# Kernel optimization log

Hardware: AMD Instinct MI355X
Metric: run time of the kernel (lower is better)

The kernel has to match this reference:

```python
import jax, jax.numpy as jnp
import numpy as np

N = 20000   # nodes per graph batch
E = 160000  # edges
G = 128     # graphs in batch
F = 114     # node feature dim (num_features == num_features_xd)
H = 10      # GAT heads
HF = F * H  # 1140


def setup_inputs() -> dict:
    key = jax.random.key(0)
    ks = jax.random.split(key, 64)
    ki = iter(range(64))
    def rn(shape, scale=0.05):
        return jax.random.normal(ks[next(ki)], shape, dtype=jnp.float32) * scale
    inp = {}
    inp["x1"] = jax.random.normal(ks[next(ki)], (N, F), dtype=jnp.float32)
    inp["edge_index1"] = jax.random.randint(ks[next(ki)], (2, E), 0, N)
    inp["batch1"] = jnp.sort(jax.random.randint(ks[next(ki)], (N,), 0, G))
    inp["x2"] = jax.random.normal(ks[next(ki)], (N, F), dtype=jnp.float32)
    inp["edge_index2"] = jax.random.randint(ks[next(ki)], (2, E), 0, N)
    inp["batch2"] = jnp.sort(jax.random.randint(ks[next(ki)], (N,), 0, G))
    inp["target"] = jax.random.normal(ks[next(ki)], (G, 1000), dtype=jnp.float32)
    for p in ("p1", "p2"):
        inp[p + "_gatW"] = rn((F, HF))
        inp[p + "_att_src"] = rn((H, F))
        inp[p + "_att_dst"] = rn((H, F))
        inp[p + "_gatb"] = rn((HF,))
        inp[p + "_gcnW"] = rn((HF, HF))
        inp[p + "_gcnb"] = rn((HF,))
        inp[p + "_fcg1W"] = rn((2 * HF, 1000))
        inp[p + "_fcg1b"] = rn((1000,))
        inp[p + "_fcg2W"] = rn((1000, 64))
        inp[p + "_fcg2b"] = rn((64,))
    inp["fcxtW"] = rn((1000, 128)); inp["fcxtb"] = rn((128,))
    inp["fc1W"] = rn((256, 128)); inp["fc1b"] = rn((128,))
    inp["fc2W"] = rn((128, 32)); inp["fc2b"] = rn((32,))
    inp["outW"] = rn((32, 1)); inp["outb"] = rn((1,))
    return inp


def lrelu(v):
    return jax.nn.leaky_relu(v, 0.01)  # nn.LeakyReLU default slope


def gat_conv(x, src, dst, W, att_src, att_dst, b):
    # PyG GATConv (concat heads, add_self_loops handled by caller)
    h = (x @ W).reshape(N, H, F)                     # [N,H,F]
    a_s = jnp.sum(h * att_src[None], axis=-1)        # [N,H]
    a_d = jnp.sum(h * att_dst[None], axis=-1)        # [N,H]
    e = jax.nn.leaky_relu(a_s[src] + a_d[dst], 0.2)  # [E',H]
    m = jax.ops.segment_max(e, dst, num_segments=N)
    ex = jnp.exp(e - m[dst])
    den = jax.ops.segment_sum(ex, dst, num_segments=N)
    alpha = ex / den[dst]                            # softmax over incoming edges
    out = jax.ops.segment_sum(alpha[:, :, None] * h[src], dst, num_segments=N)
    return out.reshape(N, HF) + b


def gcn_conv(x, src, dst, W, b):
    # PyG GCNConv with self loops (added by caller), symmetric normalization
    deg = jax.ops.segment_sum(jnp.ones_like(dst, dtype=x.dtype), dst, num_segments=N)
    dinv = jax.lax.rsqrt(jnp.maximum(deg, 1.0))
    h = x @ W                                        # [N,HF]
    msg = (dinv[src] * dinv[dst])[:, None] * h[src]
    return jax.ops.segment_sum(msg, dst, num_segments=N) + b


def branch(x, edge_index, batch, gatW, a_s, a_d, gatb, gcnW, gcnb, f1W, f1b, f2W, f2b):
    loop = jnp.arange(N, dtype=edge_index.dtype)
    src = jnp.concatenate([edge_index[0], loop])
    dst = jnp.concatenate([edge_index[1], loop])
    h = lrelu(gat_conv(x, src, dst, gatW, a_s, a_d, gatb))
    h = lrelu(gcn_conv(h, src, dst, gcnW, gcnb))
    mx = jax.ops.segment_max(h, batch, num_segments=G)
    mx = jnp.where(jnp.isfinite(mx), mx, 0.0)        # guard empty graphs
    cnt = jax.ops.segment_sum(jnp.ones((N,), h.dtype), batch, num_segments=G)
    mean = jax.ops.segment_sum(h, batch, num_segments=G) / jnp.maximum(cnt, 1.0)[:, None]
    g = jnp.concatenate([mx, mean], axis=1)          # [G, 2*HF]
    g = lrelu(g @ f1W + f1b)                         # dropout is identity at eval
    return g @ f2W + f2b                             # [G, 64]


def reference(x1, edge_index1, batch1, x2, edge_index2, batch2, target,
              p1_gatW, p1_att_src, p1_att_dst, p1_gatb, p1_gcnW, p1_gcnb,
              p1_fcg1W, p1_fcg1b, p1_fcg2W, p1_fcg2b,
              p2_gatW, p2_att_src, p2_att_dst, p2_gatb, p2_gcnW, p2_gcnb,
              p2_fcg1W, p2_fcg1b, p2_fcg2W, p2_fcg2b,
              fcxtW, fcxtb, fc1W, fc1b, fc2W, fc2b, outW, outb):
    g1 = branch(x1, edge_index1, batch1, p1_gatW, p1_att_src, p1_att_dst, p1_gatb,
                p1_gcnW, p1_gcnb, p1_fcg1W, p1_fcg1b, p1_fcg2W, p1_fcg2b)
    g2 = branch(x2, edge_index2, batch2, p2_gatW, p2_att_src, p2_att_dst, p2_gatb,
                p2_gcnW, p2_gcnb, p2_fcg1W, p2_fcg1b, p2_fcg2W, p2_fcg2b)
    xd = jnp.concatenate([g1, g2], axis=1)           # [G,128]
    xt = target.reshape(-1, 1000) @ fcxtW + fcxtb    # [G,128]
    xc = jnp.concatenate([xd, xt], axis=1)           # [G,256]
    xc = lrelu(xc @ fc1W + fc1b)
    xc = lrelu(xc @ fc2W + fc2b)
    return xc @ outW + outb                          # [G,1]
```

## Files before the change

### kernel.cpp

```cpp
#include <hip/hip_runtime.h>
#include <cstddef>
#include <cstdint>

#define NN 20000
#define EE 160000
#define EPRIME 180000
#define GG 128
#define FF 114
#define HH 10
#define HFD 1140
#define KP 1152
#define F1K 2280
#define F1KS 18
#define F1KC 128
#define NSCB 79

typedef unsigned short ushort_t;
typedef __attribute__((ext_vector_type(8))) short bf16x8;
typedef __attribute__((ext_vector_type(4))) float f32x4;

static constexpr size_t REL  = (size_t)NN * KP;
static constexpr size_t ZREL = (size_t)10 * NN * 128;

static inline int cdiv(int a, int b) { return (a + b - 1) / b; }


__device__ __forceinline__ ushort_t f2bf(float v) {
    union { float f; unsigned u; } c; c.f = v;
    unsigned u = c.u;
    unsigned r = (u + 0x7fffu + ((u >> 16) & 1u)) >> 16;
    return (ushort_t)r;
}
__device__ __forceinline__ float bf2f(ushort_t h) {
    union { unsigned u; float f; } c; c.u = ((unsigned)h) << 16;
    return c.f;
}

__device__ __forceinline__ void gload16(const void* g, const ushort_t* l) {
    __builtin_amdgcn_global_load_lds(
        (const __attribute__((address_space(1))) unsigned int*)g,
        (__attribute__((address_space(3))) unsigned int*)l, 16, 0, 0);
}


__global__ void k_init(int* __restrict__ deg, int* __restrict__ gstart, int* __restrict__ gend) {
    int br = blockIdx.y;
    int i = blockIdx.x * blockDim.x + threadIdx.x;
    if (i < NN) deg[br * NN + i] = 1;
    if (i < GG) { gstart[br * GG + i] = NN; gend[br * GG + i] = 0; }
}

__global__ void k_count(const int* __restrict__ ei0, const int* __restrict__ ei1,
                        int* __restrict__ deg) {
    int br = blockIdx.y;
    const int* ei = br ? ei1 : ei0;
    int i = blockIdx.x * blockDim.x + threadIdx.x;
    if (i < EE) atomicAdd(&deg[br * NN + ei[EE + i]], 1);
}

__global__ void k_scan1(const int* __restrict__ deg, int* __restrict__ offs, int* __restrict__ bsum) {
    __shared__ int tmp[256];
    int br = blockIdx.y;
    deg += br * NN; offs += br * (NN + 1); bsum += br * 128;
    int b = blockIdx.x, tid = threadIdx.x;
    int i = b * 256 + tid;
    int v = (i < NN) ? deg[i] : 0;
    tmp[tid] = v;
    __syncthreads();
#pragma unroll
    for (int off = 1; off < 256; off <<= 1) {
        int t = (tid >= off) ? tmp[tid - off] : 0;
        __syncthreads();
        tmp[tid] += t;
        __syncthreads();
    }
    if (i < NN) offs[i + 1] = tmp[tid];
    if (tid == 255) bsum[b] = tmp[255];
}

__global__ void k_scan2(int* __restrict__ bsum) {
    __shared__ int tmp[128];
    bsum += blockIdx.y * 128;
    int tid = threadIdx.x;
    int v = (tid < NSCB) ? bsum[tid] : 0;
    tmp[tid] = v;
    __syncthreads();
#pragma unroll
    for (int off = 1; off < 128; off <<= 1) {
        int t = (tid >= off) ? tmp[tid - off] : 0;
        __syncthreads();
        tmp[tid] += t;
        __syncthreads();
    }
    if (tid < NSCB) bsum[tid] = tmp[tid] - v;
}

__global__ void k_scan3prep(int* __restrict__ offs, const int* __restrict__ bsum,
                            int* __restrict__ cursor, const int* __restrict__ deg,
                            float* __restrict__ dinv,
                            const int* __restrict__ batch0, const int* __restrict__ batch1,
                            int* __restrict__ gstart, int* __restrict__ gend) {
    int br = blockIdx.y;
    offs += br * (NN + 1); bsum += br * 128; cursor += br * NN;
    deg += br * NN; dinv += br * NN;
    const int* batch = br ? batch1 : batch0;
    gstart += br * GG; gend += br * GG;
    int i = blockIdx.x * 256 + threadIdx.x;
    if (i < NN) {
        int o = offs[i + 1] + bsum[i >> 8];
        offs[i + 1] = o;
        cursor[i] = o - deg[i];
        dinv[i] = rsqrtf((float)deg[i]);
        int b = batch[i];
        atomicMin(&gstart[b], i);
        atomicMax(&gend[b], i + 1);
    }
    if (i == 0) offs[0] = 0;
}

__global__ void k_fill(const int* __restrict__ ei0, const int* __restrict__ ei1,
                       int* __restrict__ cursor, int* __restrict__ csr) {
    int br = blockIdx.y;
    const int* ei = br ? ei1 : ei0;
    cursor += br * NN; csr += (size_t)br * EPRIME;
    int i = blockIdx.x * blockDim.x + threadIdx.x;
    if (i < EPRIME) {
        int s, d;
        if (i < EE) { s = ei[i]; d = ei[EE + i]; }
        else        { s = i - EE; d = s; }
        int pos = atomicAdd(&cursor[d], 1);
        csr[pos] = s;
    }
}


__global__ void k_split_x(const float* __restrict__ x0, const float* __restrict__ x1,
                          ushort_t* __restrict__ xb) {
    int br = blockIdx.y;
    const float* x = br ? x1 : x0;
    xb += (size_t)br * REL;
    int idx = blockIdx.x * 256 + threadIdx.x;
    if (idx >= NN * 128) return;
    int n = idx >> 7, k = idx & 127;
    float v = (k < FF) ? x[(size_t)n * FF + k] : 0.f;
    xb[idx] = f2bf(v);
}

__global__ __launch_bounds__(256) void k_tbf(const float* __restrict__ W0, const float* __restrict__ W1,
                                             int K, int Nc, int Kpad, ushort_t* __restrict__ T) {
    __shared__ float tile[64][65];
    int br = blockIdx.z;
    const float* W = br ? W1 : W0;
    T += (size_t)br * KP * KP;
    int kb = blockIdx.x * 64;
    int nb = blockIdx.y * 64;
    int c = threadIdx.x & 63, r4 = threadIdx.x >> 6;
#pragma unroll
    for (int rr = 0; rr < 16; ++rr) {
        int r = r4 * 16 + rr;
        int gk = kb + r, gn = nb + c;
        tile[r][c] = (gk < K && gn < Nc) ? W[(size_t)gk * Nc + gn] : 0.f;
    }
    __syncthreads();
#pragma unroll
    for (int rr = 0; rr < 16; ++rr) {
        int r = r4 * 16 + rr;
        int gn = nb + r, gk = kb + c;
        T[(size_t)gn * Kpad + gk] = f2bf(tile[c][r]);
    }
}

__global__ __launch_bounds__(256) void k_wgtT(const float* __restrict__ W0, const float* __restrict__ W1,
                                              ushort_t* __restrict__ WgT) {
    __shared__ float tile[64][65];
    int y = blockIdx.z;
    int br = y / 10, h = y - 10 * br;
    const float* W = br ? W1 : W0;
    ushort_t* T = WgT + ((size_t)br * 10 + h) * 128 * 128;
    int kb = blockIdx.x * 64, cb = blockIdx.y * 64;
    int c = threadIdx.x & 63, r4 = threadIdx.x >> 6;
#pragma unroll
    for (int rr = 0; rr < 16; ++rr) {
        int r = r4 * 16 + rr;
        int gk = kb + r, gc = cb + c;
        tile[r][c] = (gk < FF && gc < FF) ? W[(size_t)gk * HFD + h * FF + gc] : 0.f;
    }
    __syncthreads();
#pragma unroll
    for (int rr = 0; rr < 16; ++rr) {
        int r = r4 * 16 + rr;
        int gc2 = cb + r, gk2 = kb + c;
        T[(size_t)gc2 * 128 + gk2] = f2bf(tile[c][r]);
    }
}

__global__ void k_vsd(const float* __restrict__ W0, const float* __restrict__ W1,
                      const float* __restrict__ as0, const float* __restrict__ as1,
                      const float* __restrict__ ad0, const float* __restrict__ ad1,
                      float* __restrict__ Vs, float* __restrict__ Vd) {
    int br = blockIdx.y;
    const float* W = br ? W1 : W0;
    const float* asrc = br ? as1 : as0;
    const float* adst = br ? ad1 : ad0;
    int idx = blockIdx.x * 256 + threadIdx.x;
    if (idx >= 1280) return;
    int k = idx / 10, h = idx - 10 * (idx / 10);
    float vs = 0.f, vd = 0.f;
    if (k < FF) {
        const float* wrow = W + (size_t)k * HFD + h * FF;
        const float* s = asrc + h * FF;
        const float* d = adst + h * FF;
        for (int f = 0; f < FF; ++f) { vs += wrow[f] * s[f]; vd += wrow[f] * d[f]; }
    }
    Vs[br * 1280 + idx] = vs;
    Vd[br * 1280 + idx] = vd;
}

__global__ void k_att2(const ushort_t* __restrict__ xbase,
                       const float* __restrict__ Vs, const float* __restrict__ Vd,
                       float* __restrict__ as_, float* __restrict__ ad_) {
    int br = blockIdx.y;
    const ushort_t* xb = xbase + (size_t)br * REL;
    const float* vs = Vs + br * 1280;
    const float* vd = Vd + br * 1280;
    as_ += (size_t)br * NN * HH; ad_ += (size_t)br * NN * HH;
    int id = blockIdx.x * blockDim.x + threadIdx.x;
    if (id >= NN * HH) return;
    int n = id / HH, h = id - HH * (id / HH);
    const ushort_t* row = xb + (size_t)n * 128;
    float as = 0.f, ad = 0.f;
    for (int k = 0; k < FF; k += 2) {
        unsigned qq = *(const unsigned*)(row + k);
        float v0 = bf2f((ushort_t)(qq & 0xffffu));
        float v1 = bf2f((ushort_t)(qq >> 16));
        as += v0 * vs[k * 10 + h] + v1 * vs[(k + 1) * 10 + h];
        ad += v0 * vd[k * 10 + h] + v1 * vd[(k + 1) * 10 + h];
    }
    as_[id] = as;
    ad_[id] = ad;
}


template <int NU>
__device__ __forceinline__ void gax_grp(
    int eg, int end, int lane, float my_ad,
    const int* __restrict__ csr, const float* __restrict__ as_,
    const ushort_t* __restrict__ xb,
    float& den, float acc[HH][2]) {
    int s[NU]; float ex[NU];
#pragma unroll
    for (int u = 0; u < NU; ++u) {
        int idx = eg + u; if (idx > end - 1) idx = end - 1;
        s[u] = csr[idx];
    }
#pragma unroll
    for (int u = 0; u < NU; ++u) {
        float e = 0.f;
        if (lane < HH) {
            float t = as_[s[u] * HH + lane] + my_ad;
            t = (t >= 0.f) ? t : 0.2f * t;
            e = __expf(t);
            if (eg + u >= end) e = 0.f;
        }
        ex[u] = e;
        den += e;
    }
    unsigned xv[NU];
#pragma unroll
    for (int u = 0; u < NU; ++u)
        xv[u] = *(const unsigned*)(xb + (size_t)s[u] * 128 + 2 * lane);
#pragma unroll
    for (int u = 0; u < NU; ++u) {
        float x0 = bf2f((ushort_t)(xv[u] & 0xffffu));
        float x1 = bf2f((ushort_t)(xv[u] >> 16));
#pragma unroll
        for (int h = 0; h < HH; ++h) {
            float w = __shfl(ex[u], h, 64);
            acc[h][0] += w * x0;
            acc[h][1] += w * x1;
        }
    }
}

__global__ __launch_bounds__(256) void gat_aggx(
    const ushort_t* __restrict__ xbase,
    const float* __restrict__ as_, const float* __restrict__ ad_,
    const int* __restrict__ offs, const int* __restrict__ csr,
    ushort_t* __restrict__ Z) {
    int br = blockIdx.y;
    const ushort_t* xb = xbase + (size_t)br * REL;
    as_ += (size_t)br * NN * HH; ad_ += (size_t)br * NN * HH;
    offs += br * (NN + 1); csr += (size_t)br * EPRIME;
    ushort_t* Zb = Z + (size_t)br * ZREL;

    int lane = threadIdx.x & 63;
    int n = blockIdx.x * 4 + (threadIdx.x >> 6);
    if (n >= NN) return;
    int beg = offs[n], end = offs[n + 1];
    float my_ad = (lane < HH) ? ad_[n * HH + lane] : 0.f;

    float den = 0.f;
    float acc[HH][2];
#pragma unroll
    for (int h = 0; h < HH; ++h) { acc[h][0] = 0.f; acc[h][1] = 0.f; }

    int eg = beg;
    for (; eg + 8 <= end; eg += 8)
        gax_grp<8>(eg, end, lane, my_ad, csr, as_, xb, den, acc);
    for (; eg < end; eg += 4)
        gax_grp<4>(eg, end, lane, my_ad, csr, as_, xb, den, acc);

#pragma unroll
    for (int h = 0; h < HH; ++h) {
        float d = __shfl(den, h, 64);
        float inv = 1.f / d;
        unsigned pk = (unsigned)f2bf(acc[h][0] * inv)
                    | ((unsigned)f2bf(acc[h][1] * inv) << 16);
        *(unsigned*)(Zb + ((size_t)h * NN + n) * 128 + 2 * lane) = pk;
    }
}


__global__ __launch_bounds__(256) void mfma_hgemm(
    const ushort_t* __restrict__ Zbase, const ushort_t* __restrict__ WgT,
    const float* __restrict__ b0, const float* __restrict__ b1,
    ushort_t* __restrict__ Cbase) {
    __shared__ __align__(16) ushort_t lds[2 * 8192];
    int y = blockIdx.y;
    int br = y / 10, h = y - 10 * br;
    const ushort_t* A = Zbase + (size_t)br * ZREL + (size_t)h * NN * 128;
    const ushort_t* Bt = WgT + ((size_t)br * 10 + h) * 128 * 128;
    const float* bias = (br ? b1 : b0) + h * FF;
    ushort_t* Cb = Cbase + (size_t)br * REL;

    const int tid = threadIdx.x;
    const int lane = tid & 63;
    const int w = tid >> 6;
    const int wr = w >> 1, wc = w & 1;

    int nwg = gridDim.x;
    int q = nwg >> 3, r8 = nwg & 7;
    int xcd = blockIdx.x & 7, sidx = blockIdx.x >> 3;
    int wg = (xcd < r8 ? xcd * (q + 1) : r8 * (q + 1) + (xcd - r8) * q) + sidx;

    int row0 = wg * 128; if (row0 > NN - 128) row0 = NN - 128;

    f32x4 acc[4][4];
#pragma unroll
    for (int i = 0; i < 4; ++i)
#pragma unroll
        for (int j = 0; j < 4; ++j) acc[i][j] = (f32x4){0.f, 0.f, 0.f, 0.f};

    const char* pA[2]; const char* pB[2];
    unsigned ldsoff[2];
#pragma unroll
    for (int i = 0; i < 2; ++i) {
        int c = (w * 2 + i) * 64 + lane;
        int kg = c >> 7, r = c & 127;
        pA[i] = (const char*)A + (size_t)(row0 + r) * 256 + kg * 16;
        pB[i] = (const char*)Bt + (size_t)r * 256 + kg * 16;
        ldsoff[i] = (w * 2 + i) * 512;
    }
    const int kgf = lane >> 4, r15 = lane & 15;

    auto STAGE = [&](int buf, int ks) {
        size_t kb = (size_t)ks * 64;
        unsigned bo = buf ? 8192u : 0u;
#pragma unroll
        for (int i = 0; i < 2; ++i) {
            gload16(pA[i] + kb, lds + bo + 0 + ldsoff[i]);
            gload16(pB[i] + kb, lds + bo + 4096 + ldsoff[i]);
        }
    };

    STAGE(0, 0);
    asm volatile("s_waitcnt vmcnt(0)" ::: "memory");
    __syncthreads();
    int cur = 0;

    for (int ks = 0; ks < 4; ++ks) {
        if (ks + 1 < 4) STAGE(cur ^ 1, ks + 1);
        const ushort_t* lb = lds + (cur ? 8192u : 0u);
        bf16x8 ah[4], bh[4];
#pragma unroll
        for (int i = 0; i < 4; ++i) {
            int ra = wr * 64 + i * 16 + r15;
            int rb = wc * 64 + i * 16 + r15;
            ah[i] = *(const bf16x8*)(lb + 0 + kgf * 1024 + ra * 8);
            bh[i] = *(const bf16x8*)(lb + 4096 + kgf * 1024 + rb * 8);
        }
#pragma unroll
        for (int i = 0; i < 4; ++i)
#pragma unroll
            for (int j = 0; j < 4; ++j)
                acc[i][j] = __builtin_amdgcn_mfma_f32_16x16x32_bf16(ah[i], bh[j], acc[i][j], 0, 0, 0);
        asm volatile("s_waitcnt vmcnt(0)" ::: "memory");
        __syncthreads();
        cur ^= 1;
    }

    const int g4 = lane >> 4;
#pragma unroll
    for (int i = 0; i < 4; ++i)
#pragma unroll
        for (int j = 0; j < 4; ++j) {
            int c = wc * 64 + j * 16 + r15;
#pragma unroll
            for (int reg = 0; reg < 4; ++reg) {
                int r = row0 + wr * 64 + i * 16 + g4 * 4 + reg;
                int gc = h * FF + c;
                if (c < FF) {
                    float v = acc[i][j][reg] + bias[c];
                    v = (v >= 0.f) ? v : 0.01f * v;
                    Cb[(size_t)r * KP + gc] = f2bf(v);
                } else if (h == 9 && gc < KP) {
                    Cb[(size_t)r * KP + gc] = 0;
                }
            }
        }
}


__global__ __launch_bounds__(256) void mfma_gemm(
    const ushort_t* __restrict__ Abase, const ushort_t* __restrict__ Btbase,
    int lda, int ldb, int M, int Nreal, int ksteps, int ncb,
    ushort_t* __restrict__ Cbase, int ldcs) {
    __shared__ __align__(16) ushort_t lds[3 * 8192];
    const int br = blockIdx.y;
    const ushort_t* A = Abase + (size_t)br * REL;
    const ushort_t* Bt = Btbase + (size_t)br * KP * KP;
    ushort_t* Cb = Cbase + (size_t)br * ZREL;

    const int tid = threadIdx.x;
    const int lane = tid & 63;
    const int w = tid >> 6;
    const int wr = w >> 1, wc = w & 1;

    int nwg = gridDim.x;
    int q = nwg >> 3, r8 = nwg & 7;
    int xcd = blockIdx.x & 7, sidx = blockIdx.x >> 3;
    int wg = (xcd < r8 ? xcd * (q + 1) : r8 * (q + 1) + (xcd - r8) * q) + sidx;
    int brow = wg / ncb, bcol = wg - brow * ncb;

    int row0 = brow * 128; if (row0 > M - 128) row0 = M - 128;
    const int col0 = bcol * 128;

    f32x4 acc[4][4];
#pragma unroll
    for (int i = 0; i < 4; ++i)
#pragma unroll
        for (int j = 0; j < 4; ++j) acc[i][j] = (f32x4){0.f, 0.f, 0.f, 0.f};

    const size_t ldaB = (size_t)lda * 2, ldbB = (size_t)ldb * 2;
    const char* pA[2]; const char* pB[2];
    unsigned ldsoff[2];
#pragma unroll
    for (int i = 0; i < 2; ++i) {
        int c = (w * 2 + i) * 64 + lane;
        int kg = c >> 7, r = c & 127;
        pA[i] = (const char*)A + (size_t)(row0 + r) * ldaB + kg * 16;
        pB[i] = (const char*)Bt + (size_t)(col0 + r) * ldbB + kg * 16;
        ldsoff[i] = (w * 2 + i) * 512;
    }
    const int kgf = lane >> 4, r15 = lane & 15;

    auto STAGE = [&](int stg, int ks) {
        size_t kb = (size_t)ks * 64;
        unsigned bo = (unsigned)stg * 8192u;
#pragma unroll
        for (int i = 0; i < 2; ++i) {
            gload16(pA[i] + kb, lds + bo + 0 + ldsoff[i]);
            gload16(pB[i] + kb, lds + bo + 4096 + ldsoff[i]);
        }
    };

    STAGE(0, 0);
    STAGE(1, 1);
    asm volatile("s_waitcnt vmcnt(4)" ::: "memory");
    __builtin_amdgcn_s_barrier();
    __builtin_amdgcn_sched_barrier(0);

    for (int ks = 0; ks < ksteps; ++ks) {
        if (ks + 2 < ksteps) STAGE((ks + 2) % 3, ks + 2);
        const ushort_t* lb = lds + (ks % 3) * 8192;
        bf16x8 ah[4], bh[4];
#pragma unroll
        for (int i = 0; i < 4; ++i) {
            int ra = wr * 64 + i * 16 + r15;
            int rb = wc * 64 + i * 16 + r15;
            ah[i] = *(const bf16x8*)(lb + 0 + kgf * 1024 + ra * 8);
            bh[i] = *(const bf16x8*)(lb + 4096 + kgf * 1024 + rb * 8);
        }
#pragma unroll
        for (int i = 0; i < 4; ++i)
#pragma unroll
            for (int j = 0; j < 4; ++j)
                acc[i][j] = __builtin_amdgcn_mfma_f32_16x16x32_bf16(ah[i], bh[j], acc[i][j], 0, 0, 0);
        if (ks + 2 < ksteps) { asm volatile("s_waitcnt vmcnt(4)" ::: "memory"); }
        else                 { asm volatile("s_waitcnt vmcnt(0)" ::: "memory"); }
        __builtin_amdgcn_s_barrier();
        __builtin_amdgcn_sched_barrier(0);
    }

    const int g4 = lane >> 4;
#pragma unroll
    for (int i = 0; i < 4; ++i)
#pragma unroll
        for (int j = 0; j < 4; ++j) {
            int c = col0 + wc * 64 + j * 16 + r15;
#pragma unroll
            for (int reg = 0; reg < 4; ++reg) {
                int r = row0 + wr * 64 + i * 16 + g4 * 4 + reg;
                if (r < M) {
                    float v = (c < Nreal) ? acc[i][j][reg] : 0.f;
                    Cb[(size_t)r * ldcs + c] = f2bf(v);
                }
            }
        }
}


template <int NU>
__device__ __forceinline__ void gcn_grp(
    int eg, int end, float di,
    const int* __restrict__ csr, const float* __restrict__ dinv,
    const ushort_t* __restrict__ h2s,
    float& a0, float& a1) {
    int s[NU]; float w[NU];
#pragma unroll
    for (int u = 0; u < NU; ++u) {
        int idx = eg + u; if (idx > end - 1) idx = end - 1;
        s[u] = csr[idx];
    }
#pragma unroll
    for (int u = 0; u < NU; ++u) {
        float ww = dinv[s[u]] * di;
        w[u] = (eg + u < end) ? ww : 0.f;
    }
    unsigned qv[NU];
#pragma unroll
    for (int u = 0; u < NU; ++u)
        qv[u] = *(const unsigned*)(h2s + (size_t)s[u] * KP);
#pragma unroll
    for (int u = 0; u < NU; ++u) {
        a0 += w[u] * bf2f((ushort_t)(qv[u] & 0xffffu));
        a1 += w[u] * bf2f((ushort_t)(qv[u] >> 16));
    }
}

__global__ __launch_bounds__(256) void gcn_agg(
    const ushort_t* __restrict__ h2base, const int* __restrict__ offs, const int* __restrict__ csr,
    const float* __restrict__ dinv,
    const float* __restrict__ b0, const float* __restrict__ b1,
    ushort_t* __restrict__ outbase) {
    int br = blockIdx.z;
    int tile = blockIdx.y;
    const ushort_t* h2b = h2base + (size_t)br * ZREL;
    offs += br * (NN + 1); csr += (size_t)br * EPRIME; dinv += br * NN;
    const float* bias = br ? b1 : b0;
    ushort_t* outb = outbase + (size_t)br * REL;

    int lane = threadIdx.x & 63;
    int n = blockIdx.x * 4 + (threadIdx.x >> 6);
    if (n >= NN) return;
    const int k0 = tile * 128 + 2 * lane;
    const ushort_t* h2s = h2b + k0;
    int beg = offs[n], end = offs[n + 1];
    float di = dinv[n];
    float a0 = 0.f, a1 = 0.f;

    int eg = beg;
    for (; eg + 8 <= end; eg += 8) gcn_grp<8>(eg, end, di, csr, dinv, h2s, a0, a1);
    for (; eg < end; eg += 4)      gcn_grp<4>(eg, end, di, csr, dinv, h2s, a0, a1);

    float v0 = 0.f, v1 = 0.f;
    if (k0 < HFD)     { v0 = a0 + bias[k0];     v0 = (v0 >= 0.f) ? v0 : 0.01f * v0; }
    if (k0 + 1 < HFD) { v1 = a1 + bias[k0 + 1]; v1 = (v1 >= 0.f) ? v1 : 0.01f * v1; }
    unsigned pk = (unsigned)f2bf(v0) | ((unsigned)f2bf(v1) << 16);
    *(unsigned*)(outb + (size_t)n * KP + k0) = pk;
}


__global__ void k_pool(const ushort_t* __restrict__ hbase, const int* __restrict__ gs,
                       const int* __restrict__ ge, float* __restrict__ gpool) {
    int br = blockIdx.z;
    const ushort_t* hfeat = hbase + (size_t)br * REL;
    gs += br * GG; ge += br * GG;
    float* gout = gpool + (size_t)br * GG * 2 * HFD;
    if (threadIdx.x >= 48) return;
    int g = blockIdx.x;
    int mg = blockIdx.y * 48 + threadIdx.x;
    int s = gs[g], e = ge[g];
    int cnt = e - s;
    float mx[8], sm[8];
#pragma unroll
    for (int j = 0; j < 8; ++j) { mx[j] = -1e30f; sm[j] = 0.f; }
    for (int r = s; r < e; ++r) {
        bf16x8 qv = *(const bf16x8*)(hfeat + (size_t)r * KP + 8 * mg);
#pragma unroll
        for (int j = 0; j < 8; ++j) {
            float v = bf2f((ushort_t)qv[j]);
            mx[j] = fmaxf(mx[j], v);
            sm[j] += v;
        }
    }
    float inv = (cnt > 0) ? 1.f / (float)cnt : 0.f;
#pragma unroll
    for (int j = 0; j < 8; ++j) {
        int k = 8 * mg + j;
        if (k < HFD) {
            float m = (cnt > 0) ? mx[j] : 0.f;
            gout[(size_t)g * (2 * HFD) + k] = m;
            gout[(size_t)g * (2 * HFD) + HFD + k] = sm[j] * inv;
        }
    }
}


__global__ __launch_bounds__(256) void k_fcg1_part(
    const float* __restrict__ gpool, const float* __restrict__ B0, const float* __restrict__ B1,
    float* __restrict__ p0, float* __restrict__ p1) {
    __shared__ float As[16][64 + 4];
    __shared__ float Bs[16][64 + 4];
    int br = blockIdx.y >> 1, rowblk = blockIdx.y & 1;
    const float* A = gpool + (size_t)br * GG * F1K;
    const float* B = br ? B1 : B0;
    float* part = br ? p1 : p0;
    int tid = threadIdx.x;
    int tx = tid & 15, ty = tid >> 4;
    int row0 = rowblk * 64, col0 = blockIdx.x * 64;
    int kbeg = blockIdx.z * F1KC;
    float acc[4][4] = {};
#pragma unroll 1
    for (int kt = 0; kt < F1KC / 16; ++kt) {
        int kk = kbeg + kt * 16;
#pragma unroll
        for (int l = 0; l < 4; ++l) {
            int idx = tid + 256 * l;
            int m = idx >> 4, k = idx & 15;
            int gr = row0 + m, gk = kk + k;
            As[k][m] = (gk < F1K) ? A[(size_t)gr * F1K + gk] : 0.f;
        }
#pragma unroll
        for (int l = 0; l < 4; ++l) {
            int idx = tid + 256 * l;
            int nn = idx & 63, k = idx >> 6;
            int gc = col0 + nn, gk = kk + k;
            Bs[k][nn] = (gc < 1000 && gk < F1K) ? B[(size_t)gk * 1000 + gc] : 0.f;
        }
        __syncthreads();
#pragma unroll
        for (int k = 0; k < 16; ++k) {
            float4 av = *(const float4*)&As[k][ty * 4];
            float4 bv = *(const float4*)&Bs[k][tx * 4];
            float a[4] = {av.x, av.y, av.z, av.w};
            float b[4] = {bv.x, bv.y, bv.z, bv.w};
#pragma unroll
            for (int i = 0; i < 4; ++i)
#pragma unroll
                for (int j = 0; j < 4; ++j) acc[i][j] += a[i] * b[j];
        }
        __syncthreads();
    }
    float* pc = part + (size_t)blockIdx.z * GG * 1000;
#pragma unroll
    for (int i = 0; i < 4; ++i) {
        int r = row0 + ty * 4 + i;
#pragma unroll
        for (int j = 0; j < 4; ++j) {
            int c = col0 + tx * 4 + j;
            if (c < 1000) pc[(size_t)r * 1000 + c] = acc[i][j];
        }
    }
}

__global__ void k_fcg1_red(const float* __restrict__ p0, const float* __restrict__ p1,
                           const float* __restrict__ b0, const float* __restrict__ b1,
                           float* __restrict__ fc1out) {
    int br = blockIdx.y;
    const float* part = br ? p1 : p0;
    const float* bias = br ? b1 : b0;
    float* out = fc1out + (size_t)br * GG * 1000;
    int idx = blockIdx.x * 256 + threadIdx.x;
    if (idx >= GG * 1000) return;
    float s = 0.f;
#pragma unroll
    for (int k = 0; k < F1KS; ++k) s += part[(size_t)k * GG * 1000 + idx];
    int n = idx % 1000;
    float v = s + bias[n];
    out[idx] = (v >= 0.f) ? v : 0.01f * v;
}


__global__ __launch_bounds__(256) void k_fcg2(const float* __restrict__ fc1out,
                                              const float* __restrict__ W0, const float* __restrict__ W1,
                                              const float* __restrict__ b0, const float* __restrict__ b1,
                                              float* __restrict__ bout) {
    __shared__ float part[4][64];
    int br = blockIdx.y;
    const float* in = fc1out + (size_t)br * GG * 1000;
    const float* W = br ? W1 : W0;
    const float* b = br ? b1 : b0;
    float* out = bout + (size_t)br * GG * 64;
    int g = blockIdx.x;
    int o = threadIdx.x & 63, p = threadIdx.x >> 6;
    const float* row = in + (size_t)g * 1000;
    float acc = 0.f;
    for (int k = p * 250; k < (p + 1) * 250; ++k) acc += row[k] * W[k * 64 + o];
    part[p][o] = acc;
    __syncthreads();
    if (p == 0) out[(size_t)g * 64 + o] = part[0][o] + part[1][o] + part[2][o] + part[3][o] + b[o];
}


__global__ __launch_bounds__(256) void k_final(
    const float* __restrict__ b1, const float* __restrict__ b2, const float* __restrict__ target,
    const float* __restrict__ fcxtW, const float* __restrict__ fcxtb,
    const float* __restrict__ fc1W, const float* __restrict__ fc1b,
    const float* __restrict__ fc2W, const float* __restrict__ fc2b,
    const float* __restrict__ outW, const float* __restrict__ outb,
    float* __restrict__ out) {
    __shared__ float xc[256];
    __shared__ float xt2[128];
    __shared__ float y1[128];
    __shared__ float y2[32];
    int g = blockIdx.x, t = threadIdx.x;
    if (t < 64) xc[t] = b1[(size_t)g * 64 + t];
    else if (t < 128) xc[t] = b2[(size_t)g * 64 + (t - 64)];
    {
        int c = t & 127, p = t >> 7;
        float acc = 0.f;
        const float* trow = target + (size_t)g * 1000;
        for (int k = p * 500; k < (p + 1) * 500; ++k) acc += trow[k] * fcxtW[k * 128 + c];
        if (p == 1) xt2[c] = acc;
        __syncthreads();
        if (p == 0) xc[128 + c] = acc + xt2[c] + fcxtb[c];
    }
    __syncthreads();
    if (t < 128) {
        float acc = 0.f;
        for (int k = 0; k < 256; ++k) acc += xc[k] * fc1W[k * 128 + t];
        acc += fc1b[t];
        y1[t] = (acc >= 0.f) ? acc : 0.01f * acc;
    }
    __syncthreads();
    if (t < 32) {
        float acc = 0.f;
        for (int k = 0; k < 128; ++k) acc += y1[k] * fc2W[k * 32 + t];
        acc += fc2b[t];
        y2[t] = (acc >= 0.f) ? acc : 0.01f * acc;
    }
    __syncthreads();
    if (t == 0) {
        float acc = 0.f;
        for (int k = 0; k < 32; ++k) acc += y2[k] * outW[k];
        out[g] = acc + outb[0];
    }
}


extern "C" void kernel_launch(void* const* d_in, const int* in_sizes, int n_in,
                              void* d_out, int out_size, void* d_ws, size_t ws_size,
                              hipStream_t stream) {
    (void)in_sizes; (void)n_in; (void)out_size; (void)ws_size;

    size_t off = 0;
    auto alloc = [&](size_t bytes) -> void* {
        void* p = (char*)d_ws + off;
        off += (bytes + 255) & ~(size_t)255;
        return p;
    };
    char* brA = (char*)alloc(2 * ZREL * 2);
    char* brB = (char*)alloc(2 * REL * 2);
    ushort_t* Bt  = (ushort_t*)alloc(2 * (size_t)KP * KP * 2);
    ushort_t* WgT = (ushort_t*)alloc(20 * (size_t)128 * 128 * 2);
    float* Vs     = (float*)alloc(2 * 1280 * 4);
    float* Vd     = (float*)alloc(2 * 1280 * 4);
    float* a_s    = (float*)alloc(2 * (size_t)NN * HH * 4);
    float* a_d    = (float*)alloc(2 * (size_t)NN * HH * 4);
    int*   deg    = (int*)alloc(2 * (size_t)NN * 4);
    int*   offs   = (int*)alloc(2 * (size_t)(NN + 1) * 4);
    int*   cursor = (int*)alloc(2 * (size_t)NN * 4);
    int*   csr    = (int*)alloc(2 * (size_t)EPRIME * 4);
    float* dinv   = (float*)alloc(2 * (size_t)NN * 4);
    int*   gstart = (int*)alloc(2 * (size_t)GG * 4);
    int*   gend   = (int*)alloc(2 * (size_t)GG * 4);
    int*   bsum   = (int*)alloc(2 * (size_t)128 * 4);
    float* gpool  = (float*)alloc(2 * (size_t)GG * 2 * HFD * 4);
    float* fc1out = (float*)alloc(2 * (size_t)GG * 1000 * 4);
    float* bout   = (float*)alloc(2 * (size_t)GG * 64 * 4);

    ushort_t* Zb  = (ushort_t*)brA;
    float* f1p0 = (float*)brA;
    float* f1p1 = (float*)(brA + (size_t)F1KS * GG * 1000 * 4);
    ushort_t* xb  = (ushort_t*)brB;

    const float* target = (const float*)d_in[6];
    const int NRB = cdiv(NN, 128);
    const int NCB = KP / 128;

    const float* x0 = (const float*)d_in[0];
    const float* x1 = (const float*)d_in[3];
    const int* ei0 = (const int*)d_in[1];
    const int* ei1 = (const int*)d_in[4];
    const int* batch0 = (const int*)d_in[2];
    const int* batch1 = (const int*)d_in[5];
    const float *gatW0 = (const float*)d_in[7],  *gatW1 = (const float*)d_in[17];
    const float *asrc0 = (const float*)d_in[8],  *asrc1 = (const float*)d_in[18];
    const float *adst0 = (const float*)d_in[9],  *adst1 = (const float*)d_in[19];
    const float *gatb0 = (const float*)d_in[10], *gatb1 = (const float*)d_in[20];
    const float *gcnW0 = (const float*)d_in[11], *gcnW1 = (const float*)d_in[21];
    const float *gcnb0 = (const float*)d_in[12], *gcnb1 = (const float*)d_in[22];
    const float *f1W0  = (const float*)d_in[13], *f1W1  = (const float*)d_in[23];
    const float *f1b0  = (const float*)d_in[14], *f1b1  = (const float*)d_in[24];
    const float *f2W0  = (const float*)d_in[15], *f2W1  = (const float*)d_in[25];
    const float *f2b0  = (const float*)d_in[16], *f2b1  = (const float*)d_in[26];

    hipLaunchKernelGGL(k_init, dim3(cdiv(NN, 256), 2), dim3(256), 0, stream, deg, gstart, gend);
    hipLaunchKernelGGL(k_count, dim3(cdiv(EE, 256), 2), dim3(256), 0, stream, ei0, ei1, deg);
    hipLaunchKernelGGL(k_scan1, dim3(NSCB, 2), dim3(256), 0, stream, deg, offs, bsum);
    hipLaunchKernelGGL(k_scan2, dim3(1, 2), dim3(128), 0, stream, bsum);
    hipLaunchKernelGGL(k_scan3prep, dim3(NSCB, 2), dim3(256), 0, stream,
                       offs, bsum, cursor, deg, dinv, batch0, batch1, gstart, gend);
    hipLaunchKernelGGL(k_fill, dim3(cdiv(EPRIME, 256), 2), dim3(256), 0, stream, ei0, ei1, cursor, csr);

    hipLaunchKernelGGL(k_split_x, dim3(cdiv(NN * 128, 256), 2), dim3(256), 0, stream, x0, x1, xb);
    hipLaunchKernelGGL(k_wgtT, dim3(2, 2, 20), dim3(256), 0, stream, gatW0, gatW1, WgT);
    hipLaunchKernelGGL(k_vsd, dim3(5, 2), dim3(256), 0, stream,
                       gatW0, gatW1, asrc0, asrc1, adst0, adst1, Vs, Vd);

    hipLaunchKernelGGL(k_att2, dim3(cdiv(NN * HH, 256), 2), dim3(256), 0, stream,
                       xb, Vs, Vd, a_s, a_d);

    hipLaunchKernelGGL(gat_aggx, dim3(cdiv(NN, 4), 2), dim3(256), 0, stream,
                       xb, a_s, a_d, offs, csr, Zb);

    hipLaunchKernelGGL(mfma_hgemm, dim3(NRB, 20), dim3(256), 0, stream,
                       Zb, WgT, gatb0, gatb1, xb);

    hipLaunchKernelGGL(k_tbf, dim3(KP / 64, KP / 64, 2), dim3(256), 0, stream,
                       gcnW0, gcnW1, HFD, HFD, KP, Bt);

    hipLaunchKernelGGL(mfma_gemm, dim3(NRB * NCB, 2), dim3(256), 0, stream,
                       xb, Bt, KP, KP, NN, HFD, KP / 32, NCB, Zb, KP);

    hipLaunchKernelGGL(gcn_agg, dim3(cdiv(NN, 4), 9, 2), dim3(256), 0, stream,
                       Zb, offs, csr, dinv, gcnb0, gcnb1, xb);

    hipLaunchKernelGGL(k_pool, dim3(GG, 3, 2), dim3(64), 0, stream, xb, gstart, gend, gpool);

    hipLaunchKernelGGL(k_fcg1_part, dim3(16, 4, F1KS), dim3(256), 0, stream,
                       gpool, f1W0, f1W1, f1p0, f1p1);
    hipLaunchKernelGGL(k_fcg1_red, dim3(cdiv(GG * 1000, 256), 2), dim3(256), 0, stream,
                       f1p0, f1p1, f1b0, f1b1, fc1out);

    hipLaunchKernelGGL(k_fcg2, dim3(GG, 2), dim3(256), 0, stream,
                       fc1out, f2W0, f2W1, f2b0, f2b1, bout);

    hipLaunchKernelGGL(k_final, dim3(GG), dim3(256), 0, stream,
                       bout, bout + (size_t)GG * 64, target,
                       (const float*)d_in[27], (const float*)d_in[28],
                       (const float*)d_in[29], (const float*)d_in[30],
                       (const float*)d_in[31], (const float*)d_in[32],
                       (const float*)d_in[33], (const float*)d_in[34],
                       (float*)d_out);
}
```

Before: 832.6 us.

## Enlarge GCN GEMM row tile to 256 with 512-thread blocks, double buffering

The dense GCN weight GEMM now uses 256-row by 128-column output tiles with eight waves per block instead of 128x128 tiles with four waves. This halves the number of row blocks, so each B tile loaded from global memory is reused across twice as many rows. The LDS pipeline changes from a three-stage ring with partial vmcnt waits to a two-buffer scheme that waits for all loads and runs a full __syncthreads every k-step. That can expose more global-load latency, and the larger block may lower occupancy.

Result: slower. 874.7 us (+5.1%).

```diff
diff --git a/kernel.cpp b/kernel.cpp
--- a/kernel.cpp
+++ b/kernel.cpp
@@ -421,11 +421,11 @@
 }
 
 
-__global__ __launch_bounds__(256) void mfma_gemm(
+__global__ __launch_bounds__(512) void mfma_gemm(
     const ushort_t* __restrict__ Abase, const ushort_t* __restrict__ Btbase,
     int lda, int ldb, int M, int Nreal, int ksteps, int ncb,
     ushort_t* __restrict__ Cbase, int ldcs) {
-    __shared__ __align__(16) ushort_t lds[3 * 8192];
+    __shared__ __align__(16) ushort_t lds[2 * 12288];
     const int br = blockIdx.y;
     const ushort_t* A = Abase + (size_t)br * REL;
     const ushort_t* Bt = Btbase + (size_t)br * KP * KP;
@@ -442,7 +442,7 @@
     int wg = (xcd < r8 ? xcd * (q + 1) : r8 * (q + 1) + (xcd - r8) * q) + sidx;
     int brow = wg / ncb, bcol = wg - brow * ncb;
 
-    int row0 = brow * 128; if (row0 > M - 128) row0 = M - 128;
+    int row0 = brow * 256; if (row0 > M - 256) row0 = M - 256;
     const int col0 = bcol * 128;
 
     f32x4 acc[4][4];
@@ -452,54 +452,51 @@
         for (int j = 0; j < 4; ++j) acc[i][j] = (f32x4){0.f, 0.f, 0.f, 0.f};
 
     const size_t ldaB = (size_t)lda * 2, ldbB = (size_t)ldb * 2;
-    const char* pA[2]; const char* pB[2];
-    unsigned ldsoff[2];
-#pragma unroll
-    for (int i = 0; i < 2; ++i) {
-        int c = (w * 2 + i) * 64 + lane;
-        int kg = c >> 7, r = c & 127;
-        pA[i] = (const char*)A + (size_t)(row0 + r) * ldaB + kg * 16;
-        pB[i] = (const char*)Bt + (size_t)(col0 + r) * ldbB + kg * 16;
-        ldsoff[i] = (w * 2 + i) * 512;
+    const char* pS[3];
+    unsigned ldst[3];
+#pragma unroll
+    for (int l = 0; l < 3; ++l) {
+        int c = l * 512 + tid;
+        if (c < 1024) { int kg = c >> 8, r = c & 255;
+                        pS[l] = (const char*)A + (size_t)(row0 + r) * ldaB + kg * 16; }
+        else          { int cc = c - 1024; int kg = cc >> 7, r = cc & 127;
+                        pS[l] = (const char*)Bt + (size_t)(col0 + r) * ldbB + kg * 16; }
+        ldst[l] = (unsigned)c * 8;
     }
     const int kgf = lane >> 4, r15 = lane & 15;
 
-    auto STAGE = [&](int stg, int ks) {
+    auto STAGE = [&](int buf, int ks) {
         size_t kb = (size_t)ks * 64;
-        unsigned bo = (unsigned)stg * 8192u;
-#pragma unroll
-        for (int i = 0; i < 2; ++i) {
-            gload16(pA[i] + kb, lds + bo + 0 + ldsoff[i]);
-            gload16(pB[i] + kb, lds + bo + 4096 + ldsoff[i]);
-        }
+        unsigned bo = buf ? 12288u : 0u;
+#pragma unroll
+        for (int l = 0; l < 3; ++l)
+            gload16(pS[l] + kb, lds + bo + ldst[l]);
     };
 
     STAGE(0, 0);
-    STAGE(1, 1);
-    asm volatile("s_waitcnt vmcnt(4)" ::: "memory");
-    __builtin_amdgcn_s_barrier();
-    __builtin_amdgcn_sched_barrier(0);
+    asm volatile("s_waitcnt vmcnt(0)" ::: "memory");
+    __syncthreads();
+    int cur = 0;
 
     for (int ks = 0; ks < ksteps; ++ks) {
-        if (ks + 2 < ksteps) STAGE((ks + 2) % 3, ks + 2);
-        const ushort_t* lb = lds + (ks % 3) * 8192;
+        if (ks + 1 < ksteps) STAGE(cur ^ 1, ks + 1);
+        const ushort_t* lb = lds + (cur ? 12288u : 0u);
         bf16x8 ah[4], bh[4];
 #pragma unroll
         for (int i = 0; i < 4; ++i) {
             int ra = wr * 64 + i * 16 + r15;
             int rb = wc * 64 + i * 16 + r15;
-            ah[i] = *(const bf16x8*)(lb + 0 + kgf * 1024 + ra * 8);
-            bh[i] = *(const bf16x8*)(lb + 4096 + kgf * 1024 + rb * 8);
+            ah[i] = *(const bf16x8*)(lb + kgf * 2048 + ra * 8);
+            bh[i] = *(const bf16x8*)(lb + 8192 + kgf * 1024 + rb * 8);
         }
 #pragma unroll
         for (int i = 0; i < 4; ++i)
 #pragma unroll
             for (int j = 0; j < 4; ++j)
                 acc[i][j] = __builtin_amdgcn_mfma_f32_16x16x32_bf16(ah[i], bh[j], acc[i][j], 0, 0, 0);
-        if (ks + 2 < ksteps) { asm volatile("s_waitcnt vmcnt(4)" ::: "memory"); }
-        else                 { asm volatile("s_waitcnt vmcnt(0)" ::: "memory"); }
-        __builtin_amdgcn_s_barrier();
-        __builtin_amdgcn_sched_barrier(0);
+        asm volatile("s_waitcnt vmcnt(0)" ::: "memory");
+        __syncthreads();
+        cur ^= 1;
     }
 
     const int g4 = lane >> 4;
@@ -797,6 +794,7 @@
 
     const float* target = (const float*)d_in[6];
     const int NRB = cdiv(NN, 128);
+    const int NRB2 = cdiv(NN, 256);
     const int NCB = KP / 128;
 
     const float* x0 = (const float*)d_in[0];
@@ -841,7 +839,7 @@
     hipLaunchKernelGGL(k_tbf, dim3(KP / 64, KP / 64, 2), dim3(256), 0, stream,
                        gcnW0, gcnW1, HFD, HFD, KP, Bt);
 
-    hipLaunchKernelGGL(mfma_gemm, dim3(NRB * NCB, 2), dim3(256), 0, stream,
+    hipLaunchKernelGGL(mfma_gemm, dim3(NRB2 * NCB, 2), dim3(512), 0, stream,
                        xb, Bt, KP, KP, NN, HFD, KP / 32, NCB, Zb, KP);
 
     hipLaunchKernelGGL(gcn_agg, dim3(cdiv(NN, 4), 9, 2), dim3(256), 0, stream,
```
